# Kernel tuning notes

Hardware: AMD Instinct MI355X
Metric: run time of the kernel (lower is better)

The kernel has to match this reference:

```python
import jax, jax.numpy as jnp
import numpy as np

N = 1536
F = 64          # in_features
F_IN = F + 1    # include_adj adds adjacency channel
OUT = 64


def setup_inputs() -> dict:
    key = jax.random.key(0)
    k1, k2, k3, k4 = jax.random.split(key, 4)
    feat = jax.random.normal(k1, (N, F), dtype=jnp.float32)
    adj = jax.random.uniform(k2, (N, N), dtype=jnp.float32)
    # nn.Linear init: U(-1/sqrt(fan_in), 1/sqrt(fan_in))
    bound = 1.0 / np.sqrt(F_IN)
    W = jax.random.uniform(k3, (OUT, F_IN), minval=-bound, maxval=bound, dtype=jnp.float32)
    b = jax.random.uniform(k4, (OUT,), minval=-bound, maxval=bound, dtype=jnp.float32)
    return {"feat": feat, "adj": adj, "W": W, "b": b}


def reference(feat, adj, W, b):
    # pairwise abs-diff via broadcasting (no repeat): [N, N, F]
    feat_diff = jnp.abs(feat[None, :, :] - feat[:, None, :])
    # concat adjacency as extra channel -> [N, N, F+1], then flatten rows
    x = jnp.concatenate([feat_diff, adj[:, :, None]], axis=2).reshape(N * N, F_IN)
    # Linear: x @ W.T + b -> [N*N, OUT]
    return x @ W.T + b
```

## Files before the change

### kernel.cpp

```cpp
#include <hip/hip_runtime.h>
#include <hip/hip_bf16.h>

#define N_NODES 1536
#define NF 64
#define NOUT 64
#define FIN 65
#define TI 8

typedef __bf16 bf16x8 __attribute__((ext_vector_type(8)));
typedef float f32x4 __attribute__((ext_vector_type(4)));

__global__ __launch_bounds__(256, 3)
void edge_gcn_mfma(const float* __restrict__ feat,
                   const float* __restrict__ adj,
                   const float* __restrict__ W,
                   const float* __restrict__ b,
                   float* __restrict__ out)
{
    const int tid  = threadIdx.x;
    const int lane = tid & 63;
    const int wv   = tid >> 6;
    const int l15  = lane & 15;
    const int lg   = lane >> 4;

    const int i0 = blockIdx.y * TI;
    const int j0 = blockIdx.x * 128;
    const int jw = j0 + wv * 32;

    __shared__ float lds[8192];

    bf16x8 afrag[2][4];
#pragma unroll
    for (int kk = 0; kk < 2; ++kk) {
#pragma unroll
        for (int mo = 0; mo < 4; ++mo) {
            const float* wp = W + (mo * 16 + l15) * FIN + kk * 32 + lg * 8;
#pragma unroll
            for (int e = 0; e < 8; ++e) afrag[kk][mo][e] = (__bf16)wp[e];
        }
    }

    float fjr[2][2][8];
#pragma unroll
    for (int n = 0; n < 2; ++n) {
        const float* fjrow = feat + (jw + n * 16 + l15) * NF;
#pragma unroll
        for (int kk = 0; kk < 2; ++kk)
#pragma unroll
            for (int e = 0; e < 8; ++e)
                fjr[n][kk][e] = fjrow[kk * 32 + lg * 8 + e];
    }

    float wl[4][4], bv[4][4];
#pragma unroll
    for (int mo = 0; mo < 4; ++mo) {
        const float* bp = b + mo * 16 + lg * 4;
#pragma unroll
        for (int r = 0; r < 4; ++r) {
            bv[mo][r] = bp[r];
            wl[mo][r] = W[(mo * 16 + lg * 4 + r) * FIN + NF];
        }
    }

    for (int ii = 0; ii < TI; ++ii) {
        const int i = i0 + ii;
        float* lbase = lds + wv * 2048;

        float fi[2][8];
#pragma unroll
        for (int kk = 0; kk < 2; ++kk) {
            const float* fp = feat + i * NF + kk * 32 + lg * 8;
#pragma unroll
            for (int e = 0; e < 8; ++e) fi[kk][e] = fp[e];
        }

        f32x4 acc[4][2];
#pragma unroll
        for (int mo = 0; mo < 4; ++mo)
#pragma unroll
            for (int n = 0; n < 2; ++n)
#pragma unroll
                for (int r = 0; r < 4; ++r)
                    acc[mo][n][r] = bv[mo][r];

#pragma unroll
        for (int n = 0; n < 2; ++n) {
#pragma unroll
            for (int kk = 0; kk < 2; ++kk) {
                bf16x8 bfrag;
#pragma unroll
                for (int e = 0; e < 8; ++e)
                    bfrag[e] = (__bf16)fabsf(fjr[n][kk][e] - fi[kk][e]);
#pragma unroll
                for (int mo = 0; mo < 4; ++mo)
                    acc[mo][n] = __builtin_amdgcn_mfma_f32_16x16x32_bf16(
                        afrag[kk][mo], bfrag, acc[mo][n], 0, 0, 0);
            }
        }

#pragma unroll
        for (int n = 0; n < 2; ++n) {
            const int jrow = n * 16 + l15;
            const float av = adj[(size_t)i * N_NODES + jw + jrow];
#pragma unroll
            for (int mo = 0; mo < 4; ++mo) {
                f32x4 v;
#pragma unroll
                for (int r = 0; r < 4; ++r)
                    v[r] = acc[mo][n][r] + av * wl[mo][r];
                const int swz = (mo * 16 + lg * 4) ^ ((l15 & 7) << 2);
                *reinterpret_cast<f32x4*>(lbase + jrow * 64 + swz) = v;
            }
        }

#pragma unroll
        for (int t = 0; t < 8; ++t) {
            const int jr = t * 4 + (lane >> 4);
            const int oo = (lane & 15) * 4;
            f32x4 v = *reinterpret_cast<const f32x4*>(
                lbase + jr * 64 + (oo ^ ((jr & 7) << 2)));
            float* op = out + ((size_t)i * N_NODES + jw + jr) * NOUT + oo;
            *reinterpret_cast<f32x4*>(op) = v;
        }
    }
}

extern "C" void kernel_launch(void* const* d_in, const int* in_sizes, int n_in,
                              void* d_out, int out_size, void* d_ws, size_t ws_size,
                              hipStream_t stream) {
    const float* feat = (const float*)d_in[0];
    const float* adj  = (const float*)d_in[1];
    const float* W    = (const float*)d_in[2];
    const float* b    = (const float*)d_in[3];
    float* out = (float*)d_out;

    dim3 grid(N_NODES / 128, N_NODES / TI);
    dim3 block(256);
    edge_gcn_mfma<<<grid, block, 0, stream>>>(feat, adj, W, b, out);
}
```

Baseline: 149.7 us.

## Software-pipeline global stores behind next row's MFMA compute via register double-buffering

The per-row loop is split into compute-to-LDS, LDS-read into registers, and global-store stages. Stores for row i are now issued after the MFMA compute of row i+1, using two register buffers, so store latency overlaps with compute. Launch bounds drop to 2 blocks per CU so the extra 64 live registers fit, which gives up occupancy. The output is a write-bound stream, so the overlap may matter less than the lost occupancy.

```diff
diff --git a/kernel.cpp b/kernel.cpp
--- a/kernel.cpp
+++ b/kernel.cpp
@@ -10,7 +10,7 @@
 typedef __bf16 bf16x8 __attribute__((ext_vector_type(8)));
 typedef float f32x4 __attribute__((ext_vector_type(4)));
 
-__global__ __launch_bounds__(256, 3)
+__global__ __launch_bounds__(256, 2)
 void edge_gcn_mfma(const float* __restrict__ feat,
                    const float* __restrict__ adj,
                    const float* __restrict__ W,
@@ -28,6 +28,7 @@
     const int jw = j0 + wv * 32;
 
     __shared__ float lds[8192];
+    float* const lbase = lds + wv * 2048;
 
     bf16x8 afrag[2][4];
 #pragma unroll
@@ -62,10 +63,7 @@
         }
     }
 
-    for (int ii = 0; ii < TI; ++ii) {
-        const int i = i0 + ii;
-        float* lbase = lds + wv * 2048;
-
+    auto compute_to_lds = [&](int i) {
         float fi[2][8];
 #pragma unroll
         for (int kk = 0; kk < 2; ++kk) {
@@ -112,17 +110,36 @@
                 *reinterpret_cast<f32x4*>(lbase + jrow * 64 + swz) = v;
             }
         }
+    };
 
+    auto ds_read_tile = [&](f32x4* R) {
 #pragma unroll
         for (int t = 0; t < 8; ++t) {
-            const int jr = t * 4 + (lane >> 4);
-            const int oo = (lane & 15) * 4;
-            f32x4 v = *reinterpret_cast<const f32x4*>(
+            const int jr = t * 4 + lg;
+            const int oo = l15 * 4;
+            R[t] = *reinterpret_cast<const f32x4*>(
                 lbase + jr * 64 + (oo ^ ((jr & 7) << 2)));
-            float* op = out + ((size_t)i * N_NODES + jw + jr) * NOUT + oo;
-            *reinterpret_cast<f32x4*>(op) = v;
         }
+    };
+
+    auto store_tile = [&](const f32x4* R, int i) {
+        float* const orow = out + ((size_t)i * N_NODES + jw) * NOUT + l15 * 4;
+#pragma unroll
+        for (int t = 0; t < 8; ++t)
+            *reinterpret_cast<f32x4*>(orow + (t * 4 + lg) * NOUT) = R[t];
+    };
+
+    f32x4 Ra[8], Rb[8];
+    for (int ii = 0; ii < TI; ii += 2) {
+        compute_to_lds(i0 + ii);
+        if (ii) store_tile(Rb, i0 + ii - 1);
+        ds_read_tile(Ra);
+
+        compute_to_lds(i0 + ii + 1);
+        store_tile(Ra, i0 + ii);
+        ds_read_tile(Rb);
     }
+    store_tile(Rb, i0 + TI - 1);
 }
 
 extern "C" void kernel_launch(void* const* d_in, const int* in_sizes, int n_in,
```

Result: slower. 153.4 us (+2.5%).
